# Optimization experiments

Hardware: AMD Instinct MI355X
Metric: run time of the kernel (lower is better)

The kernel has to match this reference:

```python
import jax, jax.numpy as jnp
import numpy as np

L, B, H, A = 2048, 64, 1024, 3  # max_len, batch, hidden_size, affect dims

def setup_inputs() -> dict:
    key = jax.random.key(0)
    k1, k2, k3, k4 = jax.random.split(key, 4)
    hidden = jax.random.normal(k1, (1, B, H), dtype=jnp.float32)
    encoder_outputs = jax.random.normal(k2, (L, B, H), dtype=jnp.float32)
    embedding = jax.random.normal(k3, (L, B, A), dtype=jnp.float32)
    # nn.Parameter init: uniform(-0.01, 0.01)
    affect_matrix = jax.random.uniform(k4, (H, A), dtype=jnp.float32, minval=-0.01, maxval=0.01)
    return {"hidden": hidden, "encoder_outputs": encoder_outputs,
            "embedding": embedding, "affect_matrix": affect_matrix}

def reference(hidden, encoder_outputs, embedding, affect_matrix):
    # hidden: [1, B, H]; encoder_outputs: [L, B, H]; embedding: [L, B, 3]
    h = hidden[0]  # [B, H]
    # dot score: e[b, i] = h[b] . enc[i, b]
    dot_scores = jnp.einsum('bh,lbh->bl', h, encoder_outputs)
    # affect score: e[b, i] += h[b]^T @ affect_matrix @ emb[i, b]
    affect_scores = jnp.einsum('bk,lbk->bl', h @ affect_matrix, embedding)
    attn_energies = dot_scores + affect_scores  # [B, L]
    # F.softmax on 2D tensor (legacy default) softmaxes over dim=1
    attn = jax.nn.softmax(attn_energies, axis=-1)
    return attn[:, None, :]  # [B, 1, L]
```

## Files before the change

### kernel.cpp

```cpp
#include <hip/hip_runtime.h>
#include <math.h>

#define Lc 2048
#define Bc 64
#define Hc 1024

__global__ __launch_bounds__(256) void energy_kernel(const float* __restrict__ hidden,
                                                     const float* __restrict__ enc,
                                                     float* __restrict__ energies) {
    int wid  = threadIdx.x >> 6;
    int lane = threadIdx.x & 63;
    int r = blockIdx.x * 4 + wid;
    int b = r & (Bc - 1);
    int l = r >> 6;

    const float4* __restrict__ erow = (const float4*)(enc + (size_t)r * Hc);
    const float4* __restrict__ hrow = (const float4*)(hidden + (size_t)b * Hc);

    float acc = 0.f;
#pragma unroll
    for (int i = 0; i < 4; ++i) {
        float4 e = erow[i * 64 + lane];
        float4 h = hrow[i * 64 + lane];
        acc += e.x * h.x + e.y * h.y + e.z * h.z + e.w * h.w;
    }
    for (int off = 1; off < 64; off <<= 1) acc += __shfl_xor(acc, off);

    if (lane == 0) energies[(size_t)b * Lc + l] = acc;
}

__global__ __launch_bounds__(256) void softmax_kernel(const float* __restrict__ hidden,
                                                      const float* __restrict__ emb,
                                                      const float* __restrict__ am,
                                                      const float* __restrict__ energies,
                                                      float* __restrict__ out) {
    int b = blockIdx.x;
    int t = threadIdx.x;
    int wave = t >> 6;

    float s0 = 0.f, s1 = 0.f, s2 = 0.f;
#pragma unroll
    for (int i = 0; i < 4; ++i) {
        int h = t + i * 256;
        float hv = hidden[b * Hc + h];
        s0 += hv * am[h * 3 + 0];
        s1 += hv * am[h * 3 + 1];
        s2 += hv * am[h * 3 + 2];
    }
    for (int off = 1; off < 64; off <<= 1) {
        s0 += __shfl_xor(s0, off);
        s1 += __shfl_xor(s1, off);
        s2 += __shfl_xor(s2, off);
    }
    __shared__ float red[3][4];
    if ((t & 63) == 0) { red[0][wave] = s0; red[1][wave] = s1; red[2][wave] = s2; }
    __syncthreads();
    float ha0 = red[0][0] + red[0][1] + red[0][2] + red[0][3];
    float ha1 = red[1][0] + red[1][1] + red[1][2] + red[1][3];
    float ha2 = red[2][0] + red[2][1] + red[2][2] + red[2][3];
    __syncthreads();

    const float* row = energies + (size_t)b * Lc;
    float vals[8];
    float m = -INFINITY;
#pragma unroll
    for (int i = 0; i < 8; ++i) {
        int ll = t + i * 256;
        const float* em = emb + ((size_t)ll * Bc + b) * 3;
        float e = row[ll] + ha0 * em[0] + ha1 * em[1] + ha2 * em[2];
        vals[i] = e;
        m = fmaxf(m, e);
    }
    __shared__ float sred[4];
    for (int off = 1; off < 64; off <<= 1) m = fmaxf(m, __shfl_xor(m, off));
    if ((t & 63) == 0) sred[wave] = m;
    __syncthreads();
    m = fmaxf(fmaxf(sred[0], sred[1]), fmaxf(sred[2], sred[3]));
    __syncthreads();

    float s = 0.f;
#pragma unroll
    for (int i = 0; i < 8; ++i) {
        vals[i] = __expf(vals[i] - m);
        s += vals[i];
    }
    for (int off = 1; off < 64; off <<= 1) s += __shfl_xor(s, off);
    if ((t & 63) == 0) sred[wave] = s;
    __syncthreads();
    s = sred[0] + sred[1] + sred[2] + sred[3];
    float inv = 1.0f / s;

#pragma unroll
    for (int i = 0; i < 8; ++i) out[(size_t)b * Lc + t + i * 256] = vals[i] * inv;
}

extern "C" void kernel_launch(void* const* d_in, const int* in_sizes, int n_in,
                              void* d_out, int out_size, void* d_ws, size_t ws_size,
                              hipStream_t stream) {
    const float* hidden = (const float*)d_in[0];
    const float* enc    = (const float*)d_in[1];
    const float* emb    = (const float*)d_in[2];
    const float* am     = (const float*)d_in[3];
    float* out = (float*)d_out;

    float* energies = (float*)d_ws;

    energy_kernel<<<(Lc * Bc) / 4, 256, 0, stream>>>(hidden, enc, energies);
    softmax_kernel<<<Bc, 256, 0, stream>>>(hidden, emb, am, energies, out);
}
```

Before: 94.37 us.

## Make energy kernel persistent with hidden reuse and register prefetch

Launches a fixed grid of 8192 waves, each processing 16 encoder rows that share the same batch index. The wave loads its hidden vector once, then double-buffers the next row's loads in registers while reducing the current one. This is meant to remove redundant hidden loads and per-block launch overhead and to keep loads in flight. The trade-off is fewer resident waves to hide memory latency.

```diff
diff --git a/kernel.cpp b/kernel.cpp
--- a/kernel.cpp
+++ b/kernel.cpp
@@ -4,29 +4,48 @@
 #define Lc 2048
 #define Bc 64
 #define Hc 1024
+#define NWAVE 8192
+#define ITERS 16
 
 __global__ __launch_bounds__(256) void energy_kernel(const float* __restrict__ hidden,
                                                      const float* __restrict__ enc,
                                                      float* __restrict__ energies) {
     int wid  = threadIdx.x >> 6;
     int lane = threadIdx.x & 63;
-    int r = blockIdx.x * 4 + wid;
-    int b = r & (Bc - 1);
-    int l = r >> 6;
+    int w    = blockIdx.x * 4 + wid;
+    int b    = w & (Bc - 1);
+    int l0   = w >> 6;
 
-    const float4* __restrict__ erow = (const float4*)(enc + (size_t)r * Hc);
     const float4* __restrict__ hrow = (const float4*)(hidden + (size_t)b * Hc);
+    float4 h0 = hrow[0 * 64 + lane];
+    float4 h1 = hrow[1 * 64 + lane];
+    float4 h2 = hrow[2 * 64 + lane];
+    float4 h3 = hrow[3 * 64 + lane];
 
-    float acc = 0.f;
-#pragma unroll
-    for (int i = 0; i < 4; ++i) {
-        float4 e = erow[i * 64 + lane];
-        float4 h = hrow[i * 64 + lane];
-        acc += e.x * h.x + e.y * h.y + e.z * h.z + e.w * h.w;
+    const float4* __restrict__ base = (const float4*)enc;
+    size_t off = (size_t)w * 256 + lane;
+    const size_t RSTRIDE = (size_t)NWAVE * 256;
+
+    float4 a0 = base[off], a1 = base[off + 64], a2 = base[off + 128], a3 = base[off + 192];
+    float4 c0 = a0, c1 = a1, c2 = a2, c3 = a3;
+
+    for (int it = 0; it < ITERS; ++it) {
+        size_t noff = off + RSTRIDE;
+        if (it < ITERS - 1) {
+            c0 = base[noff];
+            c1 = base[noff + 64];
+            c2 = base[noff + 128];
+            c3 = base[noff + 192];
+        }
+        float acc = a0.x * h0.x + a0.y * h0.y + a0.z * h0.z + a0.w * h0.w
+                  + a1.x * h1.x + a1.y * h1.y + a1.z * h1.z + a1.w * h1.w
+                  + a2.x * h2.x + a2.y * h2.y + a2.z * h2.z + a2.w * h2.w
+                  + a3.x * h3.x + a3.y * h3.y + a3.z * h3.z + a3.w * h3.w;
+        for (int o = 1; o < 64; o <<= 1) acc += __shfl_xor(acc, o);
+        if (lane == 0) energies[(size_t)b * Lc + l0 + it * 128] = acc;
+        a0 = c0; a1 = c1; a2 = c2; a3 = c3;
+        off = noff;
     }
-    for (int off = 1; off < 64; off <<= 1) acc += __shfl_xor(acc, off);
-
-    if (lane == 0) energies[(size_t)b * Lc + l] = acc;
 }
 
 __global__ __launch_bounds__(256) void softmax_kernel(const float* __restrict__ hidden,
@@ -105,6 +124,6 @@
 
     float* energies = (float*)d_ws;
 
-    energy_kernel<<<(Lc * Bc) / 4, 256, 0, stream>>>(hidden, enc, energies);
+    energy_kernel<<<NWAVE / 4, 256, 0, stream>>>(hidden, enc, energies);
     softmax_kernel<<<Bc, 256, 0, stream>>>(hidden, emb, am, energies, out);
 }
```

Result: slower. 101.6 us (+7.7%).
